# Kernel optimization log

Measured on AMD Instinct MI355X. Metric: run time of the kernel, lower is better.

Reference implementation:

```python
import jax, jax.numpy as jnp
import numpy as np

NEAR, FAR = 0.0, 6.0
N_COARSE, N_IMP = 128, 64
W = 256


def _sdf_net(p, params):
    w0, b0, w1, b1, w2, b2, w3, b3 = params
    h = jax.nn.softplus(p @ w0 + b0)
    h = jax.nn.softplus(h @ w1 + b1)
    h = jax.nn.softplus(h @ w2 + b2)
    out = h @ w3 + b3  # [..., 1 + W]
    return out[..., 0], out[..., 1:]


def _laplace_cdf(x, beta):
    # CDF of zero-mean Laplace with scale beta (VolSDF density)
    return jnp.where(x <= 0, 0.5 * jnp.exp(x / beta), 1.0 - 0.5 * jnp.exp(-x / beta))


def _sample_pdf(bins, weights, n_samples):
    # bins [R, Nc], weights [R, Nc-1] -> [R, n_samples] (deterministic, perturb=False)
    w = weights + 1e-5
    pdf = w / jnp.sum(w, -1, keepdims=True)
    cdf = jnp.concatenate([jnp.zeros_like(pdf[..., :1]), jnp.cumsum(pdf, -1)], -1)  # [R, Nc]
    u = jnp.linspace(0.0, 1.0, n_samples, dtype=bins.dtype)
    u = jnp.broadcast_to(u, (*bins.shape[:-1], n_samples))
    inds = jax.vmap(jnp.searchsorted)(cdf, u)
    below = jnp.clip(inds - 1, 0, cdf.shape[-1] - 1)
    above = jnp.clip(inds, 0, cdf.shape[-1] - 1)
    cdf_b = jnp.take_along_axis(cdf, below, -1)
    cdf_a = jnp.take_along_axis(cdf, above, -1)
    bin_b = jnp.take_along_axis(bins, below, -1)
    bin_a = jnp.take_along_axis(bins, above, -1)
    denom = jnp.where(cdf_a - cdf_b < 1e-5, 1.0, cdf_a - cdf_b)
    t = (u - cdf_b) / denom
    return bin_b + t * (bin_a - bin_b)


def _transmittance_weights(sigma, deltas):
    a = 1.0 - jnp.exp(-sigma * deltas)
    T = jnp.cumprod(jnp.concatenate([jnp.ones_like(a[..., :1]), 1.0 - a + 1e-10], -1), -1)[..., :-1]
    return a * T


def _render(rays_o, rays_d, alpha, beta, sdf_params, rad_params):
    rays_d = rays_d / jnp.linalg.norm(rays_d, axis=-1, keepdims=True)
    R = rays_o.shape[0]
    a_net = alpha[0]
    b_net = beta[0]
    t = jnp.linspace(0.0, 1.0, N_COARSE, dtype=rays_o.dtype)
    d_coarse = jnp.broadcast_to(NEAR * (1.0 - t) + FAR * t, (R, N_COARSE))

    # --- hierarchical fine sampling (torch.no_grad() in source -> stop_gradient) ---
    pts_c = rays_o[:, None, :] + rays_d[:, None, :] * d_coarse[..., None]
    sdf_c, _ = _sdf_net(pts_c, sdf_params)
    sigma_c = a_net * _laplace_cdf(-sdf_c, b_net)
    deltas_c = jnp.diff(d_coarse, axis=-1)
    w_c = _transmittance_weights(sigma_c[..., :-1], deltas_c)
    d_fine = jax.lax.stop_gradient(_sample_pdf(d_coarse, w_c, N_IMP))

    d_all = jnp.sort(jnp.concatenate([d_coarse, d_fine], -1), -1)  # [R, Nc+Nf]
    pts = rays_o[:, None, :] + rays_d[:, None, :] * d_all[..., None]

    sdf, feat = _sdf_net(pts, sdf_params)
    # analytic surface normals: nabla_p sdf(p)
    grad_fn = jax.grad(lambda p: _sdf_net(p, sdf_params)[0])
    nablas = jax.vmap(grad_fn)(pts.reshape(-1, 3)).reshape(pts.shape)
    normals = nablas / (jnp.linalg.norm(nablas, axis=-1, keepdims=True) + 1e-7)

    vdirs = jnp.broadcast_to(rays_d[:, None, :], pts.shape)
    w0, b0, w1, b1, w2, b2 = rad_params
    h = jnp.concatenate([pts, vdirs, normals, feat], -1)  # [R, Nt, 265]
    h = jax.nn.relu(h @ w0 + b0)
    h = jax.nn.relu(h @ w1 + b1)
    rgb = jax.nn.sigmoid(h @ w2 + b2)  # [R, Nt, 3]

    sigma = a_net * _laplace_cdf(-sdf, b_net)
    deltas = jnp.concatenate([jnp.diff(d_all, axis=-1), jnp.full_like(d_all[..., :1], 1e10)], -1)
    weights = _transmittance_weights(sigma, deltas)  # [R, Nt]
    rgb_map = jnp.sum(weights[..., None] * rgb, axis=-2)  # [R, 3]
    return rgb_map


def setup_inputs() -> dict:
    key = jax.random.key(0)
    ks = jax.random.split(key, 16)
    R = 2048

    def w(k, shape):
        return (jax.random.normal(k, shape, dtype=jnp.float32) / np.sqrt(shape[0])).astype(jnp.float32)

    return {
        'rays_o': jax.random.normal(ks[0], (R, 3), dtype=jnp.float32),
        'rays_d': jax.random.normal(ks[1], (R, 3), dtype=jnp.float32),
        'alpha': jnp.ones((1,), dtype=jnp.float32),
        'beta': jnp.ones((1,), dtype=jnp.float32),
        'sdf_w0': w(ks[2], (3, W)), 'sdf_b0': jnp.zeros((W,), jnp.float32),
        'sdf_w1': w(ks[3], (W, W)), 'sdf_b1': jnp.zeros((W,), jnp.float32),
        'sdf_w2': w(ks[4], (W, W)), 'sdf_b2': jnp.zeros((W,), jnp.float32),
        'sdf_w3': w(ks[5], (W, W + 1)), 'sdf_b3': jnp.zeros((W + 1,), jnp.float32),
        'rad_w0': w(ks[6], (9 + W, W)), 'rad_b0': jnp.zeros((W,), jnp.float32),
        'rad_w1': w(ks[7], (W, W)), 'rad_b1': jnp.zeros((W,), jnp.float32),
        'rad_w2': w(ks[8], (W, 3)), 'rad_b2': jnp.zeros((3,), jnp.float32),
    }


def reference(rays_o, rays_d, alpha, beta,
              sdf_w0, sdf_b0, sdf_w1, sdf_b1, sdf_w2, sdf_b2, sdf_w3, sdf_b3,
              rad_w0, rad_b0, rad_w1, rad_b1, rad_w2, rad_b2):
    sdf_params = (sdf_w0, sdf_b0, sdf_w1, sdf_b1, sdf_w2, sdf_b2, sdf_w3, sdf_b3)
    rad_params = (rad_w0, rad_b0, rad_w1, rad_b1, rad_w2, rad_b2)
    return _render(rays_o, rays_d, alpha, beta, sdf_params, rad_params)
```

## Files before the change

kernel.cpp:

```cpp
#include <hip/hip_runtime.h>
#include <math.h>

#define RAYS 2048

typedef unsigned short ushort_t;
typedef short bf16x8 __attribute__((ext_vector_type(8)));
typedef float f32x4 __attribute__((ext_vector_type(4)));

__device__ __forceinline__ float sp_act(float x) {
    return fmaxf(x, 0.0f) + log1pf(expf(-fabsf(x)));
}
__device__ __forceinline__ float lap_cdf(float x, float beta) {
    return (x <= 0.0f) ? 0.5f * expf(x / beta) : 1.0f - 0.5f * expf(-x / beta);
}
__device__ __forceinline__ float sigm(float x) { return 1.0f / (1.0f + expf(-x)); }

__device__ __forceinline__ ushort_t f2bf(float x) {
    union { float f; unsigned int u; } c; c.f = x;
    unsigned int u = c.u + 0x7FFF + ((c.u >> 16) & 1);
    return (ushort_t)(u >> 16);
}
__device__ __forceinline__ float bf2f(ushort_t s) {
    union { unsigned int u; float f; } c; c.u = ((unsigned int)s) << 16;
    return c.f;
}
__device__ __forceinline__ void split2(float v, ushort_t& hi, ushort_t& lo) {
    hi = f2bf(v);
    lo = f2bf(v - bf2f(hi));
}
template<int P>
__device__ __forceinline__ int aidx(int p, int n) { return ((n >> 3) * P + p) * 16 + (n & 7); }

__device__ __forceinline__ void mfma16x16x32(f32x4& c, bf16x8 a, bf16x8 b) {
    asm("v_mfma_f32_16x16x32_bf16 %0, %1, %2, %0" : "+v"(c) : "v"(a), "v"(b));
}

template<int MODE, int KSTEPS, bool BIAS, int PM, bool SPLIT>
__device__ __forceinline__ void mfma_gemm(const ushort_t* __restrict__ A,
                                          const ushort_t* __restrict__ Bp,
                                          const float* __restrict__ bias,
                                          ushort_t* __restrict__ OUT)
{
    constexpr int P = PM * 16;
    const int t = threadIdx.x;
    const int wave = t >> 6, lane = t & 63;
    const int r16 = lane & 15, kg = lane >> 4;
    f32x4 acc[PM][4];
#pragma unroll
    for (int m = 0; m < PM; ++m)
#pragma unroll
        for (int nf = 0; nf < 4; ++nf) acc[m][nf] = 0.0f;

#pragma unroll
    for (int ks = 0; ks < KSTEPS; ++ks) {
        bf16x8 ah[PM], al[PM], bh[4], bl[4];
#pragma unroll
        for (int m = 0; m < PM; ++m) {
            const int ab = ((ks * 4 + kg) * P + m * 16 + r16) * 16;
            ah[m] = *(const bf16x8*)(A + ab);
            if (SPLIT) al[m] = *(const bf16x8*)(A + ab + 8);
        }
#pragma unroll
        for (int nf = 0; nf < 4; ++nf) {
            const int n = wave * 64 + nf * 16 + r16;
            if (SPLIT) {
                const int bb = ((ks * 256 + n) * 4 + kg) * 16;
                bh[nf] = *(const bf16x8*)(Bp + bb);
                bl[nf] = *(const bf16x8*)(Bp + bb + 8);
            } else {
                const int bb = ((ks * 256 + n) * 4 + kg) * 8;
                bh[nf] = *(const bf16x8*)(Bp + bb);
            }
        }
#pragma unroll
        for (int m = 0; m < PM; ++m)
#pragma unroll
            for (int nf = 0; nf < 4; ++nf) {
                mfma16x16x32(acc[m][nf], ah[m], bh[nf]);
                if (SPLIT) {
                    mfma16x16x32(acc[m][nf], ah[m], bl[nf]);
                    mfma16x16x32(acc[m][nf], al[m], bh[nf]);
                }
            }
    }
#pragma unroll
    for (int nf = 0; nf < 4; ++nf) {
        const int n = wave * 64 + nf * 16 + r16;
        float bv = 0.0f;
        if (BIAS) bv = bias[n];
#pragma unroll
        for (int m = 0; m < PM; ++m) {
#pragma unroll
            for (int r = 0; r < 4; ++r) {
                const int p = m * 16 + kg * 4 + r;
                float v = acc[m][nf][r] + bv;
                if (MODE == 1) v = sp_act(v);
                if (MODE == 2) v = fmaxf(v, 0.0f);
                ushort_t hi, lo;
                split2(v, hi, lo);
                const int ob = aidx<P>(p, n);
                OUT[ob] = hi; OUT[ob + 8] = lo;
            }
        }
    }
}

template<int MODE, bool BIAS>
__device__ __forceinline__ void tile_mm(const float* __restrict__ Wm,
                                        const float* __restrict__ bias,
                                        const float* IN, float* OUT)
{
    const int t  = threadIdx.x;
    const int j0 = (t & 63) << 2;
    const int p0 = (t >> 6) << 2;
    float acc[4][4];
#pragma unroll
    for (int a = 0; a < 4; ++a)
#pragma unroll
        for (int b = 0; b < 4; ++b) acc[a][b] = 0.0f;

    for (int k = 0; k < 256; k += 4) {
        const float4 w0 = *(const float4*)(Wm + (k + 0) * 256 + j0);
        const float4 w1 = *(const float4*)(Wm + (k + 1) * 256 + j0);
        const float4 w2 = *(const float4*)(Wm + (k + 2) * 256 + j0);
        const float4 w3 = *(const float4*)(Wm + (k + 3) * 256 + j0);
#pragma unroll
        for (int pp = 0; pp < 4; ++pp) {
            const float4 av = *(const float4*)(IN + (p0 + pp) * 256 + k);
            acc[pp][0] = fmaf(av.x, w0.x, acc[pp][0]);
            acc[pp][1] = fmaf(av.x, w0.y, acc[pp][1]);
            acc[pp][2] = fmaf(av.x, w0.z, acc[pp][2]);
            acc[pp][3] = fmaf(av.x, w0.w, acc[pp][3]);
            acc[pp][0] = fmaf(av.y, w1.x, acc[pp][0]);
            acc[pp][1] = fmaf(av.y, w1.y, acc[pp][1]);
            acc[pp][2] = fmaf(av.y, w1.z, acc[pp][2]);
            acc[pp][3] = fmaf(av.y, w1.w, acc[pp][3]);
            acc[pp][0] = fmaf(av.z, w2.x, acc[pp][0]);
            acc[pp][1] = fmaf(av.z, w2.y, acc[pp][1]);
            acc[pp][2] = fmaf(av.z, w2.z, acc[pp][2]);
            acc[pp][3] = fmaf(av.z, w2.w, acc[pp][3]);
            acc[pp][0] = fmaf(av.w, w3.x, acc[pp][0]);
            acc[pp][1] = fmaf(av.w, w3.y, acc[pp][1]);
            acc[pp][2] = fmaf(av.w, w3.z, acc[pp][2]);
            acc[pp][3] = fmaf(av.w, w3.w, acc[pp][3]);
        }
    }
    float bv0 = 0.f, bv1 = 0.f, bv2 = 0.f, bv3 = 0.f;
    if constexpr (BIAS) { bv0 = bias[j0]; bv1 = bias[j0+1]; bv2 = bias[j0+2]; bv3 = bias[j0+3]; }
#pragma unroll
    for (int pp = 0; pp < 4; ++pp) {
        float r0 = acc[pp][0] + bv0;
        float r1 = acc[pp][1] + bv1;
        float r2 = acc[pp][2] + bv2;
        float r3 = acc[pp][3] + bv3;
        if constexpr (MODE == 1) { r0 = sp_act(r0); r1 = sp_act(r1); r2 = sp_act(r2); r3 = sp_act(r3); }
        if constexpr (MODE == 2) { r0 = fmaxf(r0,0.f); r1 = fmaxf(r1,0.f); r2 = fmaxf(r2,0.f); r3 = fmaxf(r3,0.f); }
        *(float4*)(OUT + (p0 + pp) * 256 + j0) = make_float4(r0, r1, r2, r3);
    }
}

__global__ __launch_bounds__(256) void prep_kernel(
    const float* __restrict__ w1, const float* __restrict__ w2, const float* __restrict__ w3,
    const float* __restrict__ rw0, const float* __restrict__ rw1,
    ushort_t* __restrict__ pw1T, ushort_t* __restrict__ pw2T, ushort_t* __restrict__ pw3T,
    ushort_t* __restrict__ pw2B, ushort_t* __restrict__ pw1B,
    ushort_t* __restrict__ pwR1, ushort_t* __restrict__ pwR0,
    float* __restrict__ w3c0)
{
    const int k = blockIdx.x, mat = blockIdx.y, n = threadIdx.x;
    const int K = (mat == 6) ? 288 : 256;
    if (k >= K) return;
    float v = 0.0f; ushort_t* dst = pw1T;
    switch (mat) {
        case 0: v = w1[k * 256 + n]; dst = pw1T; break;
        case 1: v = w2[k * 256 + n]; dst = pw2T; break;
        case 2: v = w3[k * 257 + 1 + n]; dst = pw3T;
                if (n == 0) w3c0[k] = w3[k * 257];
                break;
        case 3: v = w2[n * 256 + k]; dst = pw2B; break;
        case 4: v = w1[n * 256 + k]; dst = pw1B; break;
        case 5: v = rw1[k * 256 + n]; dst = pwR1; break;
        case 6: v = (k < 256) ? rw0[(9 + k) * 256 + n]
                  : (k < 265 ? rw0[(k - 256) * 256 + n] : 0.0f);
                dst = pwR0; break;
    }
    const int b = (((k >> 5) * 256 + n) * 4 + ((k >> 3) & 3)) * 16 + (k & 7);
    ushort_t hi, lo; split2(v, hi, lo);
    dst[b] = hi; dst[b + 8] = lo;
}

__global__ __launch_bounds__(256) void coarse_kernel(
    const float* __restrict__ rays_o, const float* __restrict__ rays_d,
    const float* __restrict__ w0, const float* __restrict__ b0,
    const float* __restrict__ w1, const float* __restrict__ b1,
    const float* __restrict__ w2, const float* __restrict__ b2,
    const float* __restrict__ w3c0, const float* __restrict__ b3,
    float* __restrict__ sdf_out)
{
    __shared__ float A[16 * 256];
    __shared__ float B[16 * 256];
    __shared__ float pts[16][3];
    const int t = threadIdx.x;
    const int base = blockIdx.x * 16;

    if (t < 16) {
        int pg = base + t;
        int ray = pg >> 7, i = pg & 127;
        float ox = rays_o[ray*3+0], oy = rays_o[ray*3+1], oz = rays_o[ray*3+2];
        float dx = rays_d[ray*3+0], dy = rays_d[ray*3+1], dz = rays_d[ray*3+2];
        float n = sqrtf(dx*dx + dy*dy + dz*dz);
        dx /= n; dy /= n; dz /= n;
        float dv = 6.0f * ((float)i / 127.0f);
        pts[t][0] = ox + dx * dv; pts[t][1] = oy + dy * dv; pts[t][2] = oz + dz * dv;
    }
    __syncthreads();
    {
        float wa = w0[t], wb = w0[256 + t], wc = w0[512 + t], bb = b0[t];
#pragma unroll
        for (int p = 0; p < 16; ++p) {
            float z = fmaf(pts[p][0], wa, fmaf(pts[p][1], wb, fmaf(pts[p][2], wc, bb)));
            A[p * 256 + t] = sp_act(z);
        }
    }
    __syncthreads();
    tile_mm<1, true>(w1, b1, A, B); __syncthreads();
    tile_mm<1, true>(w2, b2, B, A); __syncthreads();
    if (t < 16) {
        float s = b3[0];
        for (int k = 0; k < 256; ++k) s = fmaf(A[t * 256 + k], w3c0[k], s);
        sdf_out[base + t] = s;
    }
}

__global__ __launch_bounds__(256) void sample_kernel(
    const float* __restrict__ sdf_c,
    const float* __restrict__ alpha_p, const float* __restrict__ beta_p,
    float* __restrict__ d_all_g)
{
    __shared__ float sig[4][128];
    __shared__ float dc[4][128];
    __shared__ float wbuf[4][127];
    __shared__ float cdf[4][128];
    __shared__ float dfine[4][64];
    __shared__ float dall[4][192];
    const int t = threadIdx.x;
    const int wv = t >> 6, lane = t & 63;
    const int ray = blockIdx.x * 4 + wv;
    const float alpha = alpha_p[0], beta = beta_p[0];

    for (int i = lane; i < 128; i += 64) {
        float s = sdf_c[ray * 128 + i];
        sig[wv][i] = alpha * lap_cdf(-s, beta);
        dc[wv][i] = 6.0f * ((float)i / 127.0f);
    }
    __syncthreads();
    if (lane == 0) {
        float T = 1.0f, S = 0.0f;
        for (int i = 0; i < 127; ++i) {
            float delta = dc[wv][i + 1] - dc[wv][i];
            float a = 1.0f - expf(-sig[wv][i] * delta);
            float w = a * T;
            T *= (1.0f - a + 1e-10f);
            wbuf[wv][i] = w;
            S += (w + 1e-5f);
        }
        float c = 0.0f;
        cdf[wv][0] = 0.0f;
        for (int i = 0; i < 127; ++i) {
            c += (wbuf[wv][i] + 1e-5f) / S;
            cdf[wv][i + 1] = c;
        }
    }
    __syncthreads();
    {
        float u = (float)lane / 63.0f;
        int lo = 0, hi = 128;
        while (lo < hi) { int m = (lo + hi) >> 1; if (cdf[wv][m] < u) lo = m + 1; else hi = m; }
        int below = lo - 1; if (below < 0) below = 0; if (below > 127) below = 127;
        int above = lo; if (above > 127) above = 127;
        float cb = cdf[wv][below], ca = cdf[wv][above];
        float bb = dc[wv][below], ba = dc[wv][above];
        float den = ca - cb; if (den < 1e-5f) den = 1.0f;
        float tt = (u - cb) / den;
        dfine[wv][lane] = bb + tt * (ba - bb);
    }
    __syncthreads();
    {
        float v = dfine[wv][lane];
        int lo = 0, hi = 128;
        while (lo < hi) { int m = (lo + hi) >> 1; if (dc[wv][m] <= v) lo = m + 1; else hi = m; }
        dall[wv][lane + lo] = v;
    }
    for (int i = lane; i < 128; i += 64) {
        float v = dc[wv][i];
        int lo = 0, hi = 64;
        while (lo < hi) { int m = (lo + hi) >> 1; if (dfine[wv][m] < v) lo = m + 1; else hi = m; }
        dall[wv][i + lo] = v;
    }
    __syncthreads();
    for (int i = lane; i < 192; i += 64) d_all_g[ray * 192 + i] = dall[wv][i];
}

__global__ __launch_bounds__(256, 1) void fine_kernel(
    const float* __restrict__ rays_o, const float* __restrict__ rays_d,
    const float* __restrict__ dall_g,
    const float* __restrict__ w0, const float* __restrict__ b0,
    const float* __restrict__ b1, const float* __restrict__ b2, const float* __restrict__ b3,
    const ushort_t* __restrict__ pw1T, const ushort_t* __restrict__ pw2T,
    const ushort_t* __restrict__ pw3T, const ushort_t* __restrict__ pw2B,
    const ushort_t* __restrict__ pw1B,
    const ushort_t* __restrict__ pwR0, const ushort_t* __restrict__ pwR1,
    const float* __restrict__ w3c0,
    const float* __restrict__ rb0, const float* __restrict__ rb1,
    const float* __restrict__ rw2, const float* __restrict__ rb2,
    float* __restrict__ fsdf, float* __restrict__ frgb)
{
    __shared__ ushort_t buf0[16384], buf1[16384], buf2[16384];
    __shared__ ushort_t fbuf[18432];
    __shared__ float geo[32][6];
    __shared__ float red[768];
    const int t = threadIdx.x;
    const int base = blockIdx.x * 32;

    if (t < 32) {
        const int p = t, pg = base + p;
        const int ray = pg / 192, i = pg - ray * 192;
        float ox = rays_o[ray*3+0], oy = rays_o[ray*3+1], oz = rays_o[ray*3+2];
        float dx = rays_d[ray*3+0], dy = rays_d[ray*3+1], dz = rays_d[ray*3+2];
        float nm = sqrtf(dx*dx + dy*dy + dz*dz);
        dx /= nm; dy /= nm; dz /= nm;
        float dv = dall_g[ray * 192 + i];
        float px = ox + dx * dv, py = oy + dy * dv, pz = oz + dz * dv;
        geo[p][0] = px; geo[p][1] = py; geo[p][2] = pz;
        geo[p][3] = dx; geo[p][4] = dy; geo[p][5] = dz;
        ushort_t hi, lo; int ob;
        split2(px, hi, lo); ob = aidx<32>(p, 256); fbuf[ob] = hi; fbuf[ob+8] = lo;
        split2(py, hi, lo); ob = aidx<32>(p, 257); fbuf[ob] = hi; fbuf[ob+8] = lo;
        split2(pz, hi, lo); ob = aidx<32>(p, 258); fbuf[ob] = hi; fbuf[ob+8] = lo;
        split2(dx, hi, lo); ob = aidx<32>(p, 259); fbuf[ob] = hi; fbuf[ob+8] = lo;
        split2(dy, hi, lo); ob = aidx<32>(p, 260); fbuf[ob] = hi; fbuf[ob+8] = lo;
        split2(dz, hi, lo); ob = aidx<32>(p, 261); fbuf[ob] = hi; fbuf[ob+8] = lo;
    }
    for (int idx = t; idx < 32 * 23; idx += 256) {
        int p = idx & 31, k = 265 + (idx >> 5);
        const int ob = aidx<32>(p, k);
        fbuf[ob] = 0; fbuf[ob + 8] = 0;
    }
    __syncthreads();
    {
        const int n = t;
        float wa = w0[n], wb = w0[256 + n], wc = w0[512 + n], bb = b0[n];
        for (int p = 0; p < 32; ++p) {
            float z = fmaf(geo[p][0], wa, fmaf(geo[p][1], wb, fmaf(geo[p][2], wc, bb)));
            ushort_t hi, lo; split2(sp_act(z), hi, lo);
            const int ob = aidx<32>(p, n);
            buf0[ob] = hi; buf0[ob + 8] = lo;
        }
    }
    __syncthreads();
    mfma_gemm<1, 8, true, 2, true>(buf0, pw1T, b1, buf1); __syncthreads();
    mfma_gemm<1, 8, true, 2, true>(buf1, pw2T, b2, buf2); __syncthreads();
    mfma_gemm<0, 8, true, 2, true>(buf2, pw3T, b3 + 1, fbuf); __syncthreads();
    {
        const int p = t >> 3, nb = t & 7;
        float s = 0.0f;
        for (int k = nb * 32; k < nb * 32 + 32; ++k) {
            const int ob = aidx<32>(p, k);
            s = fmaf(bf2f(buf2[ob]) + bf2f(buf2[ob + 8]), w3c0[k], s);
        }
        red[t] = s;
        const int n = t;
        const float wc0 = w3c0[n];
        for (int p2 = 0; p2 < 32; ++p2) {
            const int ob = aidx<32>(p2, n);
            float h = bf2f(buf2[ob]) + bf2f(buf2[ob + 8]);
            ushort_t hi, lo; split2((1.0f - expf(-h)) * wc0, hi, lo);
            buf0[ob] = hi; buf0[ob + 8] = lo;
        }
    }
    __syncthreads();
    if (t < 32) {
        float s = b3[0];
#pragma unroll
        for (int nb = 0; nb < 8; ++nb) s += red[t * 8 + nb];
        fsdf[base + t] = s;
    }
    __syncthreads();
    mfma_gemm<0, 8, false, 2, true>(buf0, pw2B, nullptr, buf2); __syncthreads();
    {
        const int n = t;
        for (int p = 0; p < 32; ++p) {
            const int ob = aidx<32>(p, n);
            float g = bf2f(buf2[ob]) + bf2f(buf2[ob + 8]);
            float h = bf2f(buf1[ob]) + bf2f(buf1[ob + 8]);
            ushort_t hi, lo; split2(g * (1.0f - expf(-h)), hi, lo);
            buf2[ob] = hi; buf2[ob + 8] = lo;
        }
    }
    __syncthreads();
    mfma_gemm<0, 8, false, 2, true>(buf2, pw1B, nullptr, buf0); __syncthreads();
    {
        const int p = t >> 3, nb = t & 7;
        float px = geo[p][0], py = geo[p][1], pz = geo[p][2];
        float pa = 0.f, pb = 0.f, pc = 0.f;
        for (int k = nb * 32; k < nb * 32 + 32; ++k) {
            float wa = w0[k], wb = w0[256+k], wc = w0[512+k];
            float z = fmaf(px, wa, fmaf(py, wb, fmaf(pz, wc, b0[k])));
            const int ob = aidx<32>(p, k);
            float g = (bf2f(buf0[ob]) + bf2f(buf0[ob + 8])) * sigm(z);
            pa = fmaf(wa, g, pa); pb = fmaf(wb, g, pb); pc = fmaf(wc, g, pc);
        }
        red[t * 3 + 0] = pa; red[t * 3 + 1] = pb; red[t * 3 + 2] = pc;
    }
    __syncthreads();
    if (t < 32) {
        const int p = t;
        float nx = 0.f, ny = 0.f, nz = 0.f;
#pragma unroll
        for (int nb = 0; nb < 8; ++nb) {
            nx += red[(p * 8 + nb) * 3 + 0];
            ny += red[(p * 8 + nb) * 3 + 1];
            nz += red[(p * 8 + nb) * 3 + 2];
        }
        float inv = 1.0f / (sqrtf(nx*nx + ny*ny + nz*nz) + 1e-7f);
        ushort_t hi, lo; int ob;
        split2(nx * inv, hi, lo); ob = aidx<32>(p, 262); fbuf[ob] = hi; fbuf[ob+8] = lo;
        split2(ny * inv, hi, lo); ob = aidx<32>(p, 263); fbuf[ob] = hi; fbuf[ob+8] = lo;
        split2(nz * inv, hi, lo); ob = aidx<32>(p, 264); fbuf[ob] = hi; fbuf[ob+8] = lo;
    }
    __syncthreads();
    mfma_gemm<2, 9, true, 2, true>(fbuf, pwR0, rb0, buf1); __syncthreads();
    mfma_gemm<2, 8, true, 2, true>(buf1, pwR1, rb1, buf2); __syncthreads();
    {
        const int p = t >> 3, nb = t & 7;
        float s0 = 0.f, s1 = 0.f, s2 = 0.f;
        for (int k = nb * 32; k < nb * 32 + 32; ++k) {
            const int ob = aidx<32>(p, k);
            float f = bf2f(buf2[ob]) + bf2f(buf2[ob + 8]);
            s0 = fmaf(f, rw2[k*3+0], s0);
            s1 = fmaf(f, rw2[k*3+1], s1);
            s2 = fmaf(f, rw2[k*3+2], s2);
        }
        red[t * 3 + 0] = s0; red[t * 3 + 1] = s1; red[t * 3 + 2] = s2;
    }
    __syncthreads();
    if (t < 32) {
        const int p = t;
        float s0 = rb2[0], s1 = rb2[1], s2 = rb2[2];
#pragma unroll
        for (int nb = 0; nb < 8; ++nb) {
            s0 += red[(p * 8 + nb) * 3 + 0];
            s1 += red[(p * 8 + nb) * 3 + 1];
            s2 += red[(p * 8 + nb) * 3 + 2];
        }
        frgb[(base + p) * 3 + 0] = sigm(s0);
        frgb[(base + p) * 3 + 1] = sigm(s1);
        frgb[(base + p) * 3 + 2] = sigm(s2);
    }
}

__global__ __launch_bounds__(256) void composite_kernel(
    const float* __restrict__ dall_g, const float* __restrict__ fsdf,
    const float* __restrict__ frgb,
    const float* __restrict__ alpha_p, const float* __restrict__ beta_p,
    float* __restrict__ out)
{
    __shared__ float aa[4][192];
    __shared__ float da[4][192];
    const int t = threadIdx.x;
    const int wv = t >> 6, lane = t & 63;
    const int ray = blockIdx.x * 4 + wv;
    const float alpha = alpha_p[0], beta = beta_p[0];

    for (int i = lane; i < 192; i += 64) da[wv][i] = dall_g[ray * 192 + i];
    __syncthreads();
    for (int i = lane; i < 192; i += 64) {
        float s = fsdf[ray * 192 + i];
        float sg = alpha * lap_cdf(-s, beta);
        float delta = (i < 191) ? (da[wv][i + 1] - da[wv][i]) : 1e10f;
        aa[wv][i] = 1.0f - expf(-sg * delta);
    }
    __syncthreads();
    if (lane == 0) {
        float T = 1.0f, r0 = 0.f, r1 = 0.f, r2 = 0.f;
        for (int i = 0; i < 192; ++i) {
            float a = aa[wv][i];
            float w = a * T;
            T *= (1.0f - a + 1e-10f);
            const float* rp = frgb + (ray * 192 + i) * 3;
            r0 = fmaf(w, rp[0], r0);
            r1 = fmaf(w, rp[1], r1);
            r2 = fmaf(w, rp[2], r2);
        }
        out[ray * 3 + 0] = r0; out[ray * 3 + 1] = r1; out[ray * 3 + 2] = r2;
    }
}

extern "C" void kernel_launch(void* const* d_in, const int* in_sizes, int n_in,
                              void* d_out, int out_size, void* d_ws, size_t ws_size,
                              hipStream_t stream) {
    const float* rays_o = (const float*)d_in[0];
    const float* rays_d = (const float*)d_in[1];
    const float* alpha  = (const float*)d_in[2];
    const float* beta   = (const float*)d_in[3];
    const float* sw0 = (const float*)d_in[4];
    const float* sb0 = (const float*)d_in[5];
    const float* sw1 = (const float*)d_in[6];
    const float* sb1 = (const float*)d_in[7];
    const float* sw2 = (const float*)d_in[8];
    const float* sb2 = (const float*)d_in[9];
    const float* sw3 = (const float*)d_in[10];
    const float* sb3 = (const float*)d_in[11];
    const float* rw0 = (const float*)d_in[12];
    const float* rb0 = (const float*)d_in[13];
    const float* rw1 = (const float*)d_in[14];
    const float* rb1 = (const float*)d_in[15];
    const float* rw2 = (const float*)d_in[16];
    const float* rb2 = (const float*)d_in[17];

    ushort_t* wsu = (ushort_t*)d_ws;
    ushort_t* pw1T = wsu;
    ushort_t* pw2T = pw1T + 131072;
    ushort_t* pw3T = pw2T + 131072;
    ushort_t* pwR1 = pw3T + 131072;
    ushort_t* pwR0 = pwR1 + 131072;
    ushort_t* pw2B = pwR0 + 147456;
    ushort_t* pw1B = pw2B + 131072;
    float* wsf = (float*)(pw1B + 131072);
    float* w3c0  = wsf;               wsf += 256;
    float* sdf_c = wsf;               wsf += RAYS * 128;
    float* dall  = wsf;               wsf += RAYS * 192;
    float* fsdf  = wsf;               wsf += RAYS * 192;
    float* frgb  = wsf;               wsf += RAYS * 192 * 3;

    prep_kernel<<<dim3(288, 7), 256, 0, stream>>>(
        sw1, sw2, sw3, rw0, rw1, pw1T, pw2T, pw3T, pw2B, pw1B, pwR1, pwR0, w3c0);
    coarse_kernel<<<RAYS * 128 / 16, 256, 0, stream>>>(
        rays_o, rays_d, sw0, sb0, sw1, sb1, sw2, sb2, w3c0, sb3, sdf_c);
    sample_kernel<<<RAYS / 4, 256, 0, stream>>>(sdf_c, alpha, beta, dall);
    fine_kernel<<<RAYS * 192 / 32, 256, 0, stream>>>(
        rays_o, rays_d, dall,
        sw0, sb0, sb1, sb2, sb3,
        pw1T, pw2T, pw3T, pw2B, pw1B, pwR0, pwR1,
        w3c0, rb0, rb1, rw2, rb2,
        fsdf, frgb);
    composite_kernel<<<RAYS / 4, 256, 0, stream>>>(dall, fsdf, frgb, alpha, beta, (float*)d_out);
}
```

Baseline: 6.905 ms.

## Swizzle hi/lo halves in LDS activations and vectorize elementwise passes

Adds an XOR swizzle that swaps the hi and lo bf16 halves of each 16-element LDS chunk based on row bit 2, applied consistently to every reader and writer of the activation buffers. This is meant to reduce LDS bank conflicts on the MFMA A-operand loads and the epilogue stores. The elementwise passes (first layer, gradient gating steps) are also rewritten so each thread handles one 8-wide chunk with 128-bit LDS loads and stores instead of scalar per-element accesses. The risk is that any access site left unswizzled, such as the zero-fill loop, reads the wrong half, and the w0 loads in the first layer are no longer hoisted per thread.

```diff
diff --git a/kernel.cpp b/kernel.cpp
--- a/kernel.cpp
+++ b/kernel.cpp
@@ -30,6 +30,7 @@
 }
 template<int P>
 __device__ __forceinline__ int aidx(int p, int n) { return ((n >> 3) * P + p) * 16 + (n & 7); }
+__device__ __forceinline__ int hsw(int p) { return ((p >> 2) & 1) << 3; }
 
 __device__ __forceinline__ void mfma16x16x32(f32x4& c, bf16x8 a, bf16x8 b) {
     asm("v_mfma_f32_16x16x32_bf16 %0, %1, %2, %0" : "+v"(c) : "v"(a), "v"(b));
@@ -56,9 +57,11 @@
         bf16x8 ah[PM], al[PM], bh[4], bl[4];
 #pragma unroll
         for (int m = 0; m < PM; ++m) {
-            const int ab = ((ks * 4 + kg) * P + m * 16 + r16) * 16;
-            ah[m] = *(const bf16x8*)(A + ab);
-            if (SPLIT) al[m] = *(const bf16x8*)(A + ab + 8);
+            const int pa = m * 16 + r16;
+            const int ab = ((ks * 4 + kg) * P + pa) * 16;
+            const int sz = hsw(pa);
+            ah[m] = *(const bf16x8*)(A + ab + sz);
+            if (SPLIT) al[m] = *(const bf16x8*)(A + ab + (sz ^ 8));
         }
 #pragma unroll
         for (int nf = 0; nf < 4; ++nf) {
@@ -99,7 +102,8 @@
                 ushort_t hi, lo;
                 split2(v, hi, lo);
                 const int ob = aidx<P>(p, n);
-                OUT[ob] = hi; OUT[ob + 8] = lo;
+                const int sz = hsw(p);
+                OUT[ob + sz] = hi; OUT[ob + (sz ^ 8)] = lo;
             }
         }
     }
@@ -333,13 +337,14 @@
         float px = ox + dx * dv, py = oy + dy * dv, pz = oz + dz * dv;
         geo[p][0] = px; geo[p][1] = py; geo[p][2] = pz;
         geo[p][3] = dx; geo[p][4] = dy; geo[p][5] = dz;
+        const int sz = hsw(p);
         ushort_t hi, lo; int ob;
-        split2(px, hi, lo); ob = aidx<32>(p, 256); fbuf[ob] = hi; fbuf[ob+8] = lo;
-        split2(py, hi, lo); ob = aidx<32>(p, 257); fbuf[ob] = hi; fbuf[ob+8] = lo;
-        split2(pz, hi, lo); ob = aidx<32>(p, 258); fbuf[ob] = hi; fbuf[ob+8] = lo;
-        split2(dx, hi, lo); ob = aidx<32>(p, 259); fbuf[ob] = hi; fbuf[ob+8] = lo;
-        split2(dy, hi, lo); ob = aidx<32>(p, 260); fbuf[ob] = hi; fbuf[ob+8] = lo;
-        split2(dz, hi, lo); ob = aidx<32>(p, 261); fbuf[ob] = hi; fbuf[ob+8] = lo;
+        split2(px, hi, lo); ob = aidx<32>(p, 256); fbuf[ob+sz] = hi; fbuf[ob+(sz^8)] = lo;
+        split2(py, hi, lo); ob = aidx<32>(p, 257); fbuf[ob+sz] = hi; fbuf[ob+(sz^8)] = lo;
+        split2(pz, hi, lo); ob = aidx<32>(p, 258); fbuf[ob+sz] = hi; fbuf[ob+(sz^8)] = lo;
+        split2(dx, hi, lo); ob = aidx<32>(p, 259); fbuf[ob+sz] = hi; fbuf[ob+(sz^8)] = lo;
+        split2(dy, hi, lo); ob = aidx<32>(p, 260); fbuf[ob+sz] = hi; fbuf[ob+(sz^8)] = lo;
+        split2(dz, hi, lo); ob = aidx<32>(p, 261); fbuf[ob+sz] = hi; fbuf[ob+(sz^8)] = lo;
     }
     for (int idx = t; idx < 32 * 23; idx += 256) {
         int p = idx & 31, k = 265 + (idx >> 5);
@@ -347,15 +352,21 @@
         fbuf[ob] = 0; fbuf[ob + 8] = 0;
     }
     __syncthreads();
-    {
-        const int n = t;
-        float wa = w0[n], wb = w0[256 + n], wc = w0[512 + n], bb = b0[n];
-        for (int p = 0; p < 32; ++p) {
-            float z = fmaf(geo[p][0], wa, fmaf(geo[p][1], wb, fmaf(geo[p][2], wc, bb)));
+    for (int c = t; c < 1024; c += 256) {
+        const int p = c & 31, oct = c >> 5;
+        const float px = geo[p][0], py = geo[p][1], pz = geo[p][2];
+        const int sz = hsw(p);
+        bf16x8 hi8, lo8;
+#pragma unroll
+        for (int j = 0; j < 8; ++j) {
+            const int n = oct * 8 + j;
+            float z = fmaf(px, w0[n], fmaf(py, w0[256+n], fmaf(pz, w0[512+n], b0[n])));
             ushort_t hi, lo; split2(sp_act(z), hi, lo);
-            const int ob = aidx<32>(p, n);
-            buf0[ob] = hi; buf0[ob + 8] = lo;
-        }
+            hi8[j] = (short)hi; lo8[j] = (short)lo;
+        }
+        const int cb = (oct * 32 + p) * 16;
+        *(bf16x8*)(buf0 + cb + sz) = hi8;
+        *(bf16x8*)(buf0 + cb + (sz ^ 8)) = lo8;
     }
     __syncthreads();
     mfma_gemm<1, 8, true, 2, true>(buf0, pw1T, b1, buf1); __syncthreads();
@@ -363,20 +374,29 @@
     mfma_gemm<0, 8, true, 2, true>(buf2, pw3T, b3 + 1, fbuf); __syncthreads();
     {
         const int p = t >> 3, nb = t & 7;
+        const int sz = hsw(p);
         float s = 0.0f;
         for (int k = nb * 32; k < nb * 32 + 32; ++k) {
             const int ob = aidx<32>(p, k);
-            s = fmaf(bf2f(buf2[ob]) + bf2f(buf2[ob + 8]), w3c0[k], s);
+            s = fmaf(bf2f(buf2[ob + sz]) + bf2f(buf2[ob + (sz ^ 8)]), w3c0[k], s);
         }
         red[t] = s;
-        const int n = t;
-        const float wc0 = w3c0[n];
-        for (int p2 = 0; p2 < 32; ++p2) {
-            const int ob = aidx<32>(p2, n);
-            float h = bf2f(buf2[ob]) + bf2f(buf2[ob + 8]);
-            ushort_t hi, lo; split2((1.0f - expf(-h)) * wc0, hi, lo);
-            buf0[ob] = hi; buf0[ob + 8] = lo;
-        }
+    }
+    for (int c = t; c < 1024; c += 256) {
+        const int p = c & 31, oct = c >> 5;
+        const int sz = hsw(p);
+        const int cb = (oct * 32 + p) * 16;
+        bf16x8 hi8 = *(const bf16x8*)(buf2 + cb + sz);
+        bf16x8 lo8 = *(const bf16x8*)(buf2 + cb + (sz ^ 8));
+        bf16x8 ohi, olo;
+#pragma unroll
+        for (int j = 0; j < 8; ++j) {
+            float h = bf2f((ushort_t)hi8[j]) + bf2f((ushort_t)lo8[j]);
+            ushort_t hi, lo; split2((1.0f - expf(-h)) * w3c0[oct * 8 + j], hi, lo);
+            ohi[j] = (short)hi; olo[j] = (short)lo;
+        }
+        *(bf16x8*)(buf0 + cb + sz) = ohi;
+        *(bf16x8*)(buf0 + cb + (sz ^ 8)) = olo;
     }
     __syncthreads();
     if (t < 32) {
@@ -387,27 +407,37 @@
     }
     __syncthreads();
     mfma_gemm<0, 8, false, 2, true>(buf0, pw2B, nullptr, buf2); __syncthreads();
-    {
-        const int n = t;
-        for (int p = 0; p < 32; ++p) {
-            const int ob = aidx<32>(p, n);
-            float g = bf2f(buf2[ob]) + bf2f(buf2[ob + 8]);
-            float h = bf2f(buf1[ob]) + bf2f(buf1[ob + 8]);
+    for (int c = t; c < 1024; c += 256) {
+        const int p = c & 31, oct = c >> 5;
+        const int sz = hsw(p);
+        const int cb = (oct * 32 + p) * 16;
+        bf16x8 ghi = *(const bf16x8*)(buf2 + cb + sz);
+        bf16x8 glo = *(const bf16x8*)(buf2 + cb + (sz ^ 8));
+        bf16x8 hhi = *(const bf16x8*)(buf1 + cb + sz);
+        bf16x8 hlo = *(const bf16x8*)(buf1 + cb + (sz ^ 8));
+        bf16x8 ohi, olo;
+#pragma unroll
+        for (int j = 0; j < 8; ++j) {
+            float g = bf2f((ushort_t)ghi[j]) + bf2f((ushort_t)glo[j]);
+            float h = bf2f((ushort_t)hhi[j]) + bf2f((ushort_t)hlo[j]);
             ushort_t hi, lo; split2(g * (1.0f - expf(-h)), hi, lo);
-            buf2[ob] = hi; buf2[ob + 8] = lo;
-        }
+            ohi[j] = (short)hi; olo[j] = (short)lo;
+        }
+        *(bf16x8*)(buf2 + cb + sz) = ohi;
+        *(bf16x8*)(buf2 + cb + (sz ^ 8)) = olo;
     }
     __syncthreads();
     mfma_gemm<0, 8, false, 2, true>(buf2, pw1B, nullptr, buf0); __syncthreads();
     {
         const int p = t >> 3, nb = t & 7;
+        const int sz = hsw(p);
         float px = geo[p][0], py = geo[p][1], pz = geo[p][2];
         float pa = 0.f, pb = 0.f, pc = 0.f;
         for (int k = nb * 32; k < nb * 32 + 32; ++k) {
             float wa = w0[k], wb = w0[256+k], wc = w0[512+k];
             float z = fmaf(px, wa, fmaf(py, wb, fmaf(pz, wc, b0[k])));
             const int ob = aidx<32>(p, k);
-            float g = (bf2f(buf0[ob]) + bf2f(buf0[ob + 8])) * sigm(z);
+            float g = (bf2f(buf0[ob + sz]) + bf2f(buf0[ob + (sz ^ 8)])) * sigm(z);
             pa = fmaf(wa, g, pa); pb = fmaf(wb, g, pb); pc = fmaf(wc, g, pc);
         }
         red[t * 3 + 0] = pa; red[t * 3 + 1] = pb; red[t * 3 + 2] = pc;
@@ -423,20 +453,22 @@
             nz += red[(p * 8 + nb) * 3 + 2];
         }
         float inv = 1.0f / (sqrtf(nx*nx + ny*ny + nz*nz) + 1e-7f);
+        const int sz = hsw(p);
         ushort_t hi, lo; int ob;
-        split2(nx * inv, hi, lo); ob = aidx<32>(p, 262); fbuf[ob] = hi; fbuf[ob+8] = lo;
-        split2(ny * inv, hi, lo); ob = aidx<32>(p, 263); fbuf[ob] = hi; fbuf[ob+8] = lo;
-        split2(nz * inv, hi, lo); ob = aidx<32>(p, 264); fbuf[ob] = hi; fbuf[ob+8] = lo;
+        split2(nx * inv, hi, lo); ob = aidx<32>(p, 262); fbuf[ob+sz] = hi; fbuf[ob+(sz^8)] = lo;
+        split2(ny * inv, hi, lo); ob = aidx<32>(p, 263); fbuf[ob+sz] = hi; fbuf[ob+(sz^8)] = lo;
+        split2(nz * inv, hi, lo); ob = aidx<32>(p, 264); fbuf[ob+sz] = hi; fbuf[ob+(sz^8)] = lo;
     }
     __syncthreads();
     mfma_gemm<2, 9, true, 2, true>(fbuf, pwR0, rb0, buf1); __syncthreads();
     mfma_gemm<2, 8, true, 2, true>(buf1, pwR1, rb1, buf2); __syncthreads();
     {
         const int p = t >> 3, nb = t & 7;
+        const int sz = hsw(p);
         float s0 = 0.f, s1 = 0.f, s2 = 0.f;
         for (int k = nb * 32; k < nb * 32 + 32; ++k) {
             const int ob = aidx<32>(p, k);
-            float f = bf2f(buf2[ob]) + bf2f(buf2[ob + 8]);
+            float f = bf2f(buf2[ob + sz]) + bf2f(buf2[ob + (sz ^ 8)]);
             s0 = fmaf(f, rw2[k*3+0], s0);
             s1 = fmaf(f, rw2[k*3+1], s1);
             s2 = fmaf(f, rw2[k*3+2], s2);
```

Result: no change. 6.858 ms (-0.7%).
